# Kernel tuning notes

Hardware: AMD Instinct MI355X
Metric: run time of the kernel (lower is better)

Reference implementation:

```python
import jax, jax.numpy as jnp
import numpy as np

TIME = 10  # interpolation factor, hardcoded in the torch module


def _interpolation(poly, time=TIME):
    # poly: [B, M, 2] -> [B, M*time, 2]
    poly_roll = jnp.roll(poly, shift=1, axis=1)
    step = jnp.arange(time, dtype=poly.dtype) / time  # [time]
    # interp[b, m, t, c] = poly[b,m,c]*step[t] + roll[b,m,c]*(1-step[t])
    interp = (poly[:, :, None, :] * step[None, None, :, None]
              + poly_roll[:, :, None, :] * (1.0 - step)[None, None, :, None])
    B, M = poly.shape[0], poly.shape[1]
    return interp.reshape(B, M * time, 2)


def _compute_distance(pred_poly, gt_poly):
    # pred: [B, N, 2], gt: [B, G, 2] -> sq dist [B, G, N]
    diff = pred_poly[:, None, :, :] - gt_poly[:, :, None, :]
    return jnp.sum(diff * diff, axis=3)


def setup_inputs() -> dict:
    key = jax.random.key(0)
    k1, k2, k3 = jax.random.split(key, 3)
    B, N, M = 1024, 128, 128
    return {
        "ini_pred_poly": jax.random.normal(k1, (B, N, 2), dtype=jnp.float32),
        "pred_polys_": jax.random.normal(k2, (B, N, 2), dtype=jnp.float32),
        "gt_polys": jax.random.normal(k3, (B, M, 2), dtype=jnp.float32),
        "keyPointsMask": jnp.ones((B, M), dtype=jnp.float32),
    }


def reference(ini_pred_poly, pred_polys_, gt_polys, keyPointsMask):
    # ---- lossPred2NearestGt ----
    gt_interp = _interpolation(gt_polys)                     # [B, M*T, 2]
    dist_pg = _compute_distance(ini_pred_poly, gt_interp)    # [B, M*T, N]
    index_gt = jnp.argmin(dist_pg, axis=1)                   # [B, N]
    nearest_gt = jnp.take_along_axis(gt_interp, index_gt[:, :, None], axis=1)  # [B, N, 2]
    loss_pred2gt = jnp.mean(jnp.abs(pred_polys_ - nearest_gt))  # l1, mean reduction

    # ---- lossGt2NearestPred ----
    dist_gp = _compute_distance(ini_pred_poly, gt_polys)     # [B, M, N]
    index_pred = jnp.argmin(dist_gp, axis=2)                 # [B, M]
    nearest_pred = jnp.take_along_axis(pred_polys_, index_pred[:, :, None], axis=1)  # [B, M, 2]
    loss_gt2pred = jnp.abs(nearest_pred - gt_polys)          # [B, M, 2], reduction='none'

    mask = keyPointsMask[:, :, None] * jnp.ones((1, 1, 2), dtype=keyPointsMask.dtype)  # [B, M, 2]
    loss_set2set = jnp.sum(loss_gt2pred * mask) / (jnp.sum(mask) + 1.0) + loss_pred2gt
    return loss_set2set / 2.0
```

## Files before the change

kernel.cpp:

```cpp
#include <hip/hip_runtime.h>

constexpr int Bn = 1024;
constexpr int Nn = 128;
constexpr int Mn = 128;

__device__ unsigned long long g_ab[Bn];
__device__ unsigned int       g_m[Bn];
__device__ unsigned int       g_c1[64 * 16];
__device__ unsigned int       g_c2 = 0;


__global__ __launch_bounds__(256) void dm_main(
    const float2* __restrict__ ini,
    const float2* __restrict__ pred,
    const float2* __restrict__ gt,
    const float*  __restrict__ kpm,
    float* __restrict__ out)
{
    __shared__ float4 s_segA[Mn];
    __shared__ float2 s_segB[Mn];
    __shared__ float2 s_ini[Nn];
    __shared__ float2 s_pred[Nn];
    __shared__ float2 s_gt[Mn];
    __shared__ float4 s_cA[4][Nn];
    __shared__ float2 s_cB[4][Mn];
    __shared__ float  s_red[3][4];
    __shared__ bool   s_last;

    const int b   = blockIdx.x;
    const int tid = threadIdx.x;

    float kw = 0.f;
    if (tid >= Nn) kw = kpm[b*Mn + (tid - Nn)];

    if (tid < Mn) {
        const float2 cur = gt[b*Mn + tid];
        const float2 prv = gt[b*Mn + ((tid + Mn - 1) & (Mn - 1))];
        const float ex = cur.x - prv.x, ey = cur.y - prv.y;
        const float ee = fmaxf(fmaf(ex, ex, ey*ey), 1e-30f);
        const float nr = -10.0f * __builtin_amdgcn_rcpf(ee);
        s_segA[tid] = make_float4(prv.x, prv.y, ex, ey);
        s_segB[tid] = make_float2(ee, nr);
        s_gt[tid]   = cur;
    } else {
        const int t = tid - Mn;
        s_ini[t]  = ini[b*Nn + t];
        s_pred[t] = pred[b*Nn + t];
    }
    __syncthreads();

    const int lane  = tid & 63;
    const int w     = tid >> 6;
    const int mbase = w * 32;

    const float2 p0 = s_ini[lane];
    const float2 p1 = s_ini[lane + 64];
    const float2 g0 = s_gt[lane];
    const float2 g1 = s_gt[lane + 64];

    float bd0 = 3.4e38f, bd1 = 3.4e38f;
    int   bm0 = 0,       bm1 = 0;
    float bs0 = 0.f,     bs1 = 0.f;
    float cd0 = 3.4e38f, cd1 = 3.4e38f;
    int   cj0 = 0,       cj1 = 0;

    #pragma unroll 4
    for (int i = 0; i < 32; ++i) {
        const int m = mbase + i;
        const float4 A  = s_segA[m];
        const float2 Bv = s_segB[m];
        const float2 q  = s_ini[m];
        {
            const float fx = A.x - p0.x, fy = A.y - p0.y;
            const float fe = fmaf(fx, A.z, fy*A.w);
            const float ff = fmaf(fx, fx, fy*fy);
            float tv = fe * Bv.y;
            tv = fminf(fmaxf(rintf(tv), 0.f), 9.f);
            const float sp = tv * 0.1f;
            const float d  = fmaf(sp, fmaf(sp, Bv.x, fe + fe), ff);
            if (d < bd0) { bd0 = d; bm0 = m; bs0 = sp; }
        }
        {
            const float fx = A.x - p1.x, fy = A.y - p1.y;
            const float fe = fmaf(fx, A.z, fy*A.w);
            const float ff = fmaf(fx, fx, fy*fy);
            float tv = fe * Bv.y;
            tv = fminf(fmaxf(rintf(tv), 0.f), 9.f);
            const float sp = tv * 0.1f;
            const float d  = fmaf(sp, fmaf(sp, Bv.x, fe + fe), ff);
            if (d < bd1) { bd1 = d; bm1 = m; bs1 = sp; }
        }
        {
            const float dx = q.x - g0.x, dy = q.y - g0.y;
            const float d = fmaf(dx, dx, dy*dy);
            if (d < cd0) { cd0 = d; cj0 = m; }
        }
        {
            const float dx = q.x - g1.x, dy = q.y - g1.y;
            const float d = fmaf(dx, dx, dy*dy);
            if (d < cd1) { cd1 = d; cj1 = m; }
        }
    }

    s_cA[w][lane]      = make_float4(bd0, bs0, __int_as_float(bm0), 0.f);
    s_cA[w][lane + 64] = make_float4(bd1, bs1, __int_as_float(bm1), 0.f);
    s_cB[w][lane]      = make_float2(cd0, __int_as_float(cj0));
    s_cB[w][lane + 64] = make_float2(cd1, __int_as_float(cj1));
    __syncthreads();

    float sum_p2g = 0.f, sum_g2p = 0.f, sum_m = 0.f;
    if (tid < Nn) {
        const int n = tid;
        float best = 3.4e38f; float bs = 0.f; int bm = 0;
        #pragma unroll
        for (int w2 = 0; w2 < 4; ++w2) {
            const float4 c = s_cA[w2][n];
            if (c.x < best) { best = c.x; bs = c.y; bm = __float_as_int(c.z); }
        }
        const float4 A = s_segA[bm];
        const float ngx = fmaf(bs, A.z, A.x);
        const float ngy = fmaf(bs, A.w, A.y);
        const float2 pr = s_pred[n];
        sum_p2g = fabsf(pr.x - ngx) + fabsf(pr.y - ngy);
    } else {
        const int m = tid - Nn;
        float best = 3.4e38f; int nj = 0;
        #pragma unroll
        for (int w2 = 0; w2 < 4; ++w2) {
            const float2 c = s_cB[w2][m];
            if (c.x < best) { best = c.x; nj = __float_as_int(c.y); }
        }
        const float2 np_ = s_pred[nj];
        const float2 g   = s_gt[m];
        sum_g2p = kw * (fabsf(np_.x - g.x) + fabsf(np_.y - g.y));
        sum_m   = 2.0f * kw;
    }

    #pragma unroll
    for (int off = 32; off > 0; off >>= 1) {
        sum_p2g += __shfl_down(sum_p2g, off);
        sum_g2p += __shfl_down(sum_g2p, off);
        sum_m   += __shfl_down(sum_m,   off);
    }
    const int wv = tid >> 6;
    if ((tid & 63) == 0) { s_red[0][wv] = sum_p2g; s_red[1][wv] = sum_g2p; s_red[2][wv] = sum_m; }
    __syncthreads();

    if (tid == 0) {
        const float At = s_red[0][0] + s_red[0][1] + s_red[0][2] + s_red[0][3];
        const float Ct = s_red[1][0] + s_red[1][1] + s_red[1][2] + s_red[1][3];
        const float Mt = s_red[2][0] + s_red[2][1] + s_red[2][2] + s_red[2][3];
        const unsigned long long ab =
            ((unsigned long long)__float_as_uint(Ct) << 32) | __float_as_uint(At);
        __hip_atomic_store(&g_ab[b], ab, __ATOMIC_RELAXED, __HIP_MEMORY_SCOPE_AGENT);
        __hip_atomic_store(&g_m[b], __float_as_uint(Mt),
                           __ATOMIC_RELAXED, __HIP_MEMORY_SCOPE_AGENT);
        asm volatile("s_waitcnt vmcnt(0)" ::: "memory");
        bool last = false;
        const unsigned t1 = __hip_atomic_fetch_add(&g_c1[(b >> 4) << 4], 1u,
                                                   __ATOMIC_RELAXED,
                                                   __HIP_MEMORY_SCOPE_AGENT);
        if (t1 == 15u) {
            const unsigned t2 = __hip_atomic_fetch_add(&g_c2, 1u,
                                                       __ATOMIC_RELAXED,
                                                       __HIP_MEMORY_SCOPE_AGENT);
            last = (t2 == 63u);
        }
        s_last = last;
    }
    __syncthreads();
    if (!s_last) return;

    if (tid < 64) {
        __hip_atomic_store(&g_c1[tid << 4], 0u, __ATOMIC_RELAXED,
                           __HIP_MEMORY_SCOPE_AGENT);
    } else if (tid == 64) {
        __hip_atomic_store(&g_c2, 0u, __ATOMIC_RELAXED,
                           __HIP_MEMORY_SCOPE_AGENT);
    }
    float A = 0.f, C = 0.f, M = 0.f;
    #pragma unroll
    for (int k = 0; k < 4; ++k) {
        const int idx = tid + 256*k;
        const unsigned long long ab =
            __hip_atomic_load(&g_ab[idx], __ATOMIC_RELAXED, __HIP_MEMORY_SCOPE_AGENT);
        const unsigned mm =
            __hip_atomic_load(&g_m[idx], __ATOMIC_RELAXED, __HIP_MEMORY_SCOPE_AGENT);
        A += __uint_as_float((unsigned)(ab & 0xffffffffull));
        C += __uint_as_float((unsigned)(ab >> 32));
        M += __uint_as_float(mm);
    }
    #pragma unroll
    for (int off = 32; off > 0; off >>= 1) {
        A += __shfl_down(A, off); C += __shfl_down(C, off); M += __shfl_down(M, off);
    }
    __syncthreads();
    if ((tid & 63) == 0) { s_red[0][wv] = A; s_red[1][wv] = C; s_red[2][wv] = M; }
    __syncthreads();
    if (tid == 0) {
        const float At = s_red[0][0] + s_red[0][1] + s_red[0][2] + s_red[0][3];
        const float Ct = s_red[1][0] + s_red[1][1] + s_red[1][2] + s_red[1][3];
        const float Mt = s_red[2][0] + s_red[2][1] + s_red[2][2] + s_red[2][3];
        out[0] = (Ct / (Mt + 1.0f) + At * (1.0f / 262144.0f)) * 0.5f;
    }
}

extern "C" void kernel_launch(void* const* d_in, const int* in_sizes, int n_in,
                              void* d_out, int out_size, void* d_ws, size_t ws_size,
                              hipStream_t stream)
{
    const float2* ini  = (const float2*)d_in[0];
    const float2* pred = (const float2*)d_in[1];
    const float2* gt   = (const float2*)d_in[2];
    const float*  kpm  = (const float*)d_in[3];
    float* out = (float*)d_out;

    dm_main<<<Bn, 256, 0, stream>>>(ini, pred, gt, kpm, out);
}
```

Before: 72.50 us.

## Interleave segment data in LDS and make the final reduction hierarchical

Packs segment endpoints, squared length, reciprocal and ini point into two adjacent float4 entries, so the inner loop does two 128-bit LDS reads instead of three. The clamp becomes a single med3 instruction. The last block of each 16-block group now sums that group's partials into a second-level buffer, and the final block reduces 64 values in one wavefront without block-wide syncs. The trade-off is serial work for the group-finishing thread and an extra global round trip plus memory fence.

```diff
diff --git a/kernel.cpp b/kernel.cpp
--- a/kernel.cpp
+++ b/kernel.cpp
@@ -6,6 +6,8 @@
 
 __device__ unsigned long long g_ab[Bn];
 __device__ unsigned int       g_m[Bn];
+__device__ unsigned long long g2_ab[64 * 8];
+__device__ unsigned int       g2_m[64 * 16];
 __device__ unsigned int       g_c1[64 * 16];
 __device__ unsigned int       g_c2 = 0;
 
@@ -17,8 +19,7 @@
     const float*  __restrict__ kpm,
     float* __restrict__ out)
 {
-    __shared__ float4 s_segA[Mn];
-    __shared__ float2 s_segB[Mn];
+    __shared__ float4 s_seg[2 * Mn];
     __shared__ float2 s_ini[Nn];
     __shared__ float2 s_pred[Nn];
     __shared__ float2 s_gt[Mn];
@@ -33,18 +34,21 @@
     float kw = 0.f;
     if (tid >= Nn) kw = kpm[b*Mn + (tid - Nn)];
 
+    float2* s2 = reinterpret_cast<float2*>(s_seg);
     if (tid < Mn) {
         const float2 cur = gt[b*Mn + tid];
         const float2 prv = gt[b*Mn + ((tid + Mn - 1) & (Mn - 1))];
         const float ex = cur.x - prv.x, ey = cur.y - prv.y;
         const float ee = fmaxf(fmaf(ex, ex, ey*ey), 1e-30f);
         const float nr = -10.0f * __builtin_amdgcn_rcpf(ee);
-        s_segA[tid] = make_float4(prv.x, prv.y, ex, ey);
-        s_segB[tid] = make_float2(ee, nr);
+        s_seg[2*tid] = make_float4(prv.x, prv.y, ex, ey);
+        s2[4*tid + 2] = make_float2(ee, nr);
         s_gt[tid]   = cur;
     } else {
         const int t = tid - Mn;
-        s_ini[t]  = ini[b*Nn + t];
+        const float2 iv = ini[b*Nn + t];
+        s_ini[t]  = iv;
+        s2[4*t + 3] = iv;
         s_pred[t] = pred[b*Nn + t];
     }
     __syncthreads();
@@ -67,36 +71,33 @@
     #pragma unroll 4
     for (int i = 0; i < 32; ++i) {
         const int m = mbase + i;
-        const float4 A  = s_segA[m];
-        const float2 Bv = s_segB[m];
-        const float2 q  = s_ini[m];
+        const float4 A = s_seg[2*m];
+        const float4 E = s_seg[2*m + 1];
         {
             const float fx = A.x - p0.x, fy = A.y - p0.y;
             const float fe = fmaf(fx, A.z, fy*A.w);
             const float ff = fmaf(fx, fx, fy*fy);
-            float tv = fe * Bv.y;
-            tv = fminf(fmaxf(rintf(tv), 0.f), 9.f);
+            const float tv = __builtin_amdgcn_fmed3f(rintf(fe * E.y), 0.f, 9.f);
             const float sp = tv * 0.1f;
-            const float d  = fmaf(sp, fmaf(sp, Bv.x, fe + fe), ff);
+            const float d  = fmaf(sp, fmaf(sp, E.x, fe + fe), ff);
             if (d < bd0) { bd0 = d; bm0 = m; bs0 = sp; }
         }
         {
             const float fx = A.x - p1.x, fy = A.y - p1.y;
             const float fe = fmaf(fx, A.z, fy*A.w);
             const float ff = fmaf(fx, fx, fy*fy);
-            float tv = fe * Bv.y;
-            tv = fminf(fmaxf(rintf(tv), 0.f), 9.f);
+            const float tv = __builtin_amdgcn_fmed3f(rintf(fe * E.y), 0.f, 9.f);
             const float sp = tv * 0.1f;
-            const float d  = fmaf(sp, fmaf(sp, Bv.x, fe + fe), ff);
+            const float d  = fmaf(sp, fmaf(sp, E.x, fe + fe), ff);
             if (d < bd1) { bd1 = d; bm1 = m; bs1 = sp; }
         }
         {
-            const float dx = q.x - g0.x, dy = q.y - g0.y;
+            const float dx = E.z - g0.x, dy = E.w - g0.y;
             const float d = fmaf(dx, dx, dy*dy);
             if (d < cd0) { cd0 = d; cj0 = m; }
         }
         {
-            const float dx = q.x - g1.x, dy = q.y - g1.y;
+            const float dx = E.z - g1.x, dy = E.w - g1.y;
             const float d = fmaf(dx, dx, dy*dy);
             if (d < cd1) { cd1 = d; cj1 = m; }
         }
@@ -117,7 +118,7 @@
             const float4 c = s_cA[w2][n];
             if (c.x < best) { best = c.x; bs = c.y; bm = __float_as_int(c.z); }
         }
-        const float4 A = s_segA[bm];
+        const float4 A = s_seg[2*bm];
         const float ngx = fmaf(bs, A.z, A.x);
         const float ngy = fmaf(bs, A.w, A.y);
         const float2 pr = s_pred[n];
@@ -157,10 +158,31 @@
                            __ATOMIC_RELAXED, __HIP_MEMORY_SCOPE_AGENT);
         asm volatile("s_waitcnt vmcnt(0)" ::: "memory");
         bool last = false;
-        const unsigned t1 = __hip_atomic_fetch_add(&g_c1[(b >> 4) << 4], 1u,
+        const unsigned t1 = __hip_atomic_fetch_add(&g_c1[b & ~15], 1u,
                                                    __ATOMIC_RELAXED,
                                                    __HIP_MEMORY_SCOPE_AGENT);
         if (t1 == 15u) {
+            const int g = b >> 4;
+            float gA = 0.f, gC = 0.f, gM = 0.f;
+            #pragma unroll
+            for (int k = 0; k < 16; ++k) {
+                const unsigned long long v =
+                    __hip_atomic_load(&g_ab[(g << 4) + k],
+                                      __ATOMIC_RELAXED, __HIP_MEMORY_SCOPE_AGENT);
+                const unsigned mm =
+                    __hip_atomic_load(&g_m[(g << 4) + k],
+                                      __ATOMIC_RELAXED, __HIP_MEMORY_SCOPE_AGENT);
+                gA += __uint_as_float((unsigned)(v & 0xffffffffull));
+                gC += __uint_as_float((unsigned)(v >> 32));
+                gM += __uint_as_float(mm);
+            }
+            const unsigned long long gab =
+                ((unsigned long long)__float_as_uint(gC) << 32) | __float_as_uint(gA);
+            __hip_atomic_store(&g2_ab[g << 3], gab,
+                               __ATOMIC_RELAXED, __HIP_MEMORY_SCOPE_AGENT);
+            __hip_atomic_store(&g2_m[g << 4], __float_as_uint(gM),
+                               __ATOMIC_RELAXED, __HIP_MEMORY_SCOPE_AGENT);
+            asm volatile("s_waitcnt vmcnt(0)" ::: "memory");
             const unsigned t2 = __hip_atomic_fetch_add(&g_c2, 1u,
                                                        __ATOMIC_RELAXED,
                                                        __HIP_MEMORY_SCOPE_AGENT);
@@ -174,34 +196,25 @@
     if (tid < 64) {
         __hip_atomic_store(&g_c1[tid << 4], 0u, __ATOMIC_RELAXED,
                            __HIP_MEMORY_SCOPE_AGENT);
-    } else if (tid == 64) {
-        __hip_atomic_store(&g_c2, 0u, __ATOMIC_RELAXED,
-                           __HIP_MEMORY_SCOPE_AGENT);
-    }
-    float A = 0.f, C = 0.f, M = 0.f;
-    #pragma unroll
-    for (int k = 0; k < 4; ++k) {
-        const int idx = tid + 256*k;
-        const unsigned long long ab =
-            __hip_atomic_load(&g_ab[idx], __ATOMIC_RELAXED, __HIP_MEMORY_SCOPE_AGENT);
-        const unsigned mm =
-            __hip_atomic_load(&g_m[idx], __ATOMIC_RELAXED, __HIP_MEMORY_SCOPE_AGENT);
-        A += __uint_as_float((unsigned)(ab & 0xffffffffull));
-        C += __uint_as_float((unsigned)(ab >> 32));
-        M += __uint_as_float(mm);
-    }
+        if (tid == 0)
+            __hip_atomic_store(&g_c2, 0u, __ATOMIC_RELAXED,
+                               __HIP_MEMORY_SCOPE_AGENT);
+    }
+    if (tid >= 64) return;
+
+    const unsigned long long v =
+        __hip_atomic_load(&g2_ab[tid << 3], __ATOMIC_RELAXED, __HIP_MEMORY_SCOPE_AGENT);
+    const unsigned mm =
+        __hip_atomic_load(&g2_m[tid << 4], __ATOMIC_RELAXED, __HIP_MEMORY_SCOPE_AGENT);
+    float A = __uint_as_float((unsigned)(v & 0xffffffffull));
+    float C = __uint_as_float((unsigned)(v >> 32));
+    float M = __uint_as_float(mm);
     #pragma unroll
     for (int off = 32; off > 0; off >>= 1) {
         A += __shfl_down(A, off); C += __shfl_down(C, off); M += __shfl_down(M, off);
     }
-    __syncthreads();
-    if ((tid & 63) == 0) { s_red[0][wv] = A; s_red[1][wv] = C; s_red[2][wv] = M; }
-    __syncthreads();
     if (tid == 0) {
-        const float At = s_red[0][0] + s_red[0][1] + s_red[0][2] + s_red[0][3];
-        const float Ct = s_red[1][0] + s_red[1][1] + s_red[1][2] + s_red[1][3];
-        const float Mt = s_red[2][0] + s_red[2][1] + s_red[2][2] + s_red[2][3];
-        out[0] = (Ct / (Mt + 1.0f) + At * (1.0f / 262144.0f)) * 0.5f;
+        out[0] = (C / (M + 1.0f) + A * (1.0f / 262144.0f)) * 0.5f;
     }
 }
 
```

Measured after the change: 72.88 us. No clear change (+0.5%).
